# Kernel tuning notes

Measured on AMD Instinct MI355X. Metric: run time of the kernel, lower is better.

## Reference

```python
import jax, jax.numpy as jnp
import numpy as np

DIM = 48
D_STATE = 16
D_CONV = 4
EXPAND = 2
D_INNER = DIM * EXPAND          # 96
DT_RANK = (DIM + 15) // 16      # 3
EPS = 1e-5


def _interp2x_align_corners(x, axis):
    """Linear 2x upsample along one axis with align_corners=True."""
    n = x.shape[axis]
    out = 2 * n
    pos = jnp.arange(out, dtype=jnp.float32) * (n - 1) / (out - 1)
    lo = jnp.floor(pos).astype(jnp.int32)
    hi = jnp.minimum(lo + 1, n - 1)
    w = (pos - lo.astype(jnp.float32)).astype(x.dtype)
    shape = [1] * x.ndim
    shape[axis] = out
    w = w.reshape(shape)
    return jnp.take(x, lo, axis=axis) * (1 - w) + jnp.take(x, hi, axis=axis) * w


def _upsample_trilinear2x(x):
    for axis in (2, 3, 4):
        x = _interp2x_align_corners(x, axis)
    return x


def _conv3d(x, w, b, pad):
    y = jax.lax.conv_general_dilated(
        x, w, window_strides=(1, 1, 1), padding=[(pad, pad)] * 3,
        dimension_numbers=('NCDHW', 'OIDHW', 'NCDHW'))
    return y + b[None, :, None, None, None]


def _instance_norm(x):
    m = x.mean(axis=(2, 3, 4), keepdims=True)
    v = x.var(axis=(2, 3, 4), keepdims=True)  # biased var, as PyTorch InstanceNorm3d
    return (x - m) / jnp.sqrt(v + EPS)


def _mamba(u, in_proj_w, conv1d_w, conv1d_b, x_proj_w, dt_proj_w, dt_proj_b,
           A_log, D_param, out_proj_w):
    # u: (B, L, d_model)
    Bsz, L, _ = u.shape
    xz = jnp.einsum('bld,ed->ble', u, in_proj_w)        # (B, L, 2*Di)
    xi, z = jnp.split(xz, 2, axis=-1)                   # each (B, L, Di)
    # depthwise causal conv1d (pad left d_conv-1, crop to L == mamba's slice)
    xpad = jnp.pad(xi.transpose(0, 2, 1), ((0, 0), (0, 0), (D_CONV - 1, 0)))
    xc = jax.lax.conv_general_dilated(
        xpad, conv1d_w, window_strides=(1,), padding=[(0, 0)],
        dimension_numbers=('NCH', 'OIH', 'NCH'), feature_group_count=D_INNER)
    xs = jax.nn.silu((xc + conv1d_b[None, :, None]).transpose(0, 2, 1))  # (B, L, Di)

    dbc = jnp.einsum('bld,ed->ble', xs, x_proj_w)       # (B, L, dt_rank+2*N)
    dt, Bm, Cm = jnp.split(dbc, [DT_RANK, DT_RANK + D_STATE], axis=-1)
    delta = jax.nn.softplus(jnp.einsum('blr,dr->bld', dt, dt_proj_w) + dt_proj_b)

    A = -jnp.exp(A_log)                                  # (Di, N)
    dA = jnp.exp(jnp.einsum('bld,dn->bldn', delta, A))   # (B, L, Di, N)
    dBx = jnp.einsum('bld,bln->bldn', delta * xs, Bm)    # (B, L, Di, N)

    def step(h, inp):
        dA_t, dBx_t, C_t = inp                           # (B,Di,N),(B,Di,N),(B,N)
        h = dA_t * h + dBx_t
        y = jnp.einsum('bdn,bn->bd', h, C_t)
        return h, y

    h0 = jnp.zeros((Bsz, D_INNER, D_STATE), xs.dtype)
    _, ys = jax.lax.scan(step, h0,
                         (dA.transpose(1, 0, 2, 3), dBx.transpose(1, 0, 2, 3),
                          Cm.transpose(1, 0, 2)))
    y = ys.transpose(1, 0, 2) + D_param[None, None, :] * xs
    y = y * jax.nn.silu(z)
    return jnp.einsum('bld,ed->ble', y, out_proj_w)      # (B, L, d_model)


def setup_inputs() -> dict:
    key = jax.random.key(0)
    ks = jax.random.split(key, 16)
    s = 0.05
    f32 = jnp.float32
    inp = {
        'x': jax.random.normal(ks[0], (2, DIM, 12, 12, 12), f32),
        'Hx': jax.random.normal(ks[1], (2, DIM * 2, 24, 24, 24), f32),
        'W1': jax.random.normal(ks[2], (DIM, DIM * 3, 1, 1, 1), f32) * s,
        'b1': jax.random.normal(ks[3], (DIM,), f32) * s,
        'W2': jax.random.normal(ks[4], (DIM, DIM, 3, 3, 3), f32) * s,
        'b2': jax.random.normal(ks[5], (DIM,), f32) * s,
        'W3': jax.random.normal(ks[6], (DIM, DIM, 1, 1, 1), f32) * s,
        'b3': jax.random.normal(ks[7], (DIM,), f32) * s,
        'in_proj_w': jax.random.normal(ks[8], (2 * D_INNER, DIM), f32) * s,
        'conv1d_w': jax.random.normal(ks[9], (D_INNER, 1, D_CONV), f32) * s,
        'conv1d_b': jax.random.normal(ks[10], (D_INNER,), f32) * s,
        'x_proj_w': jax.random.normal(ks[11], (DT_RANK + 2 * D_STATE, D_INNER), f32) * s,
        'dt_proj_w': jax.random.normal(ks[12], (D_INNER, DT_RANK), f32) * s,
        'dt_proj_b': jax.random.normal(ks[13], (D_INNER,), f32) * 0.1,
        'A_log': jnp.log(jnp.tile(jnp.arange(1, D_STATE + 1, dtype=f32)[None, :],
                                  (D_INNER, 1))),
        'D_param': jnp.ones((D_INNER,), f32),
        'out_proj_w': jax.random.normal(ks[14], (DIM, D_INNER), f32) * s,
    }
    return inp


def reference(x, Hx, W1, b1, W2, b2, W3, b3, in_proj_w, conv1d_w, conv1d_b,
              x_proj_w, dt_proj_w, dt_proj_b, A_log, D_param, out_proj_w):
    up = _upsample_trilinear2x(x)                         # (B, dim, 2H, 2W, 2T)
    h = jnp.concatenate([up, Hx], axis=1)                 # (B, 3*dim, ...)
    h = _conv3d(h, W1, b1, 0)
    h = _conv3d(h, W2, b2, 1)
    h = _conv3d(h, W3, b3, 0)
    Lx = jax.nn.selu(_instance_norm(h))
    B, C, H, W, T = Lx.shape
    u = Lx.reshape(B, C, H * W * T).transpose(0, 2, 1)    # (B, L, C)
    ym = _mamba(u, in_proj_w, conv1d_w, conv1d_b, x_proj_w, dt_proj_w,
                dt_proj_b, A_log, D_param, out_proj_w)
    out = ym.transpose(0, 2, 1).reshape(B, C, H, W, T) + Lx
    return out
```

## Files before the change

### kernel.cpp

```cpp
#include <hip/hip_runtime.h>
#include <math.h>

#define NB 2
#define NCH 48
#define P 13824
#define DI 96
#define NSTATE 16
#define L 13824
#define CHUNK 64
#define NCK 216
#define TL 32

__device__ __forceinline__ float siluf(float x) { return x / (1.f + __expf(-x)); }
__device__ __forceinline__ float softplusf(float x) {
    return x > 0.f ? x + log1pf(expf(-x)) : log1pf(expf(x));
}

__global__ __launch_bounds__(256) void k_wtrans(const float* __restrict__ W2,
    const float* __restrict__ W1, const float* __restrict__ W3,
    const float* __restrict__ Wop, float* __restrict__ Wt, float* __restrict__ W1t,
    float* __restrict__ W3t, float* __restrict__ Wopt)
{
    int i = blockIdx.x * 256 + threadIdx.x;
    if (i < 62208) {
        int o = i / (48 * 27); int r = i % (48 * 27); int c = r / 27; int tap = r % 27;
        int og = o / 12, oi = o % 12;
        Wt[(((og * 27 + tap) * 48 + c) * 12) + oi] = W2[i];
    } else if (i < 62208 + 6912) {
        int j = i - 62208; int o = j / 144, c = j % 144;
        W1t[c * 48 + o] = W1[j];
    } else if (i < 62208 + 6912 + 2304) {
        int j = i - 62208 - 6912; int o = j / 48, c = j % 48;
        W3t[c * 48 + o] = W3[j];
    } else if (i < 62208 + 6912 + 2304 + 4608) {
        int j = i - 62208 - 6912 - 2304; int o = j / 96, q = j % 96;
        Wopt[q * 48 + o] = Wop[j];
    }
}

__global__ __launch_bounds__(128) void k_conv1(const float* __restrict__ x,
    const float* __restrict__ Hx, const float* __restrict__ W1t,
    const float* __restrict__ b1, float* __restrict__ h1)
{
    int t = blockIdx.x * 128 + threadIdx.x;
    int oh = blockIdx.y * 12;
    int b = t / P, p = t % P;
    int zi = p / 576, yi = (p / 24) % 24, xi_ = p % 24;
    float fpos; int z0, z1, y0, y1, x0, x1; float wz, wy, wx;
    fpos = (float)(zi * 11) / 23.0f; z0 = (int)floorf(fpos); wz = fpos - z0; z1 = min(z0 + 1, 11);
    fpos = (float)(yi * 11) / 23.0f; y0 = (int)floorf(fpos); wy = fpos - y0; y1 = min(y0 + 1, 11);
    fpos = (float)(xi_ * 11) / 23.0f; x0 = (int)floorf(fpos); wx = fpos - x0; x1 = min(x0 + 1, 11);
    int o000 = (z0*12+y0)*12+x0, o001 = (z0*12+y0)*12+x1;
    int o010 = (z0*12+y1)*12+x0, o011 = (z0*12+y1)*12+x1;
    int o100 = (z1*12+y0)*12+x0, o101 = (z1*12+y0)*12+x1;
    int o110 = (z1*12+y1)*12+x0, o111 = (z1*12+y1)*12+x1;
    float uz = 1.f - wz, uy = 1.f - wy, ux = 1.f - wx;
    float w000 = uz*uy*ux, w001 = uz*uy*wx, w010 = uz*wy*ux, w011 = uz*wy*wx;
    float w100 = wz*uy*ux, w101 = wz*uy*wx, w110 = wz*wy*ux, w111 = wz*wy*wx;

    float acc[12];
#pragma unroll
    for (int o = 0; o < 12; ++o) acc[o] = b1[oh + o];
    const float* xb = x + (size_t)b * 48 * 1728;
    for (int c0 = 0; c0 < 48; c0 += 4) {
        float a[4][8];
#pragma unroll
        for (int j = 0; j < 4; ++j) {
            const float* xc = xb + (c0 + j) * 1728;
            a[j][0] = xc[o000]; a[j][1] = xc[o001]; a[j][2] = xc[o010]; a[j][3] = xc[o011];
            a[j][4] = xc[o100]; a[j][5] = xc[o101]; a[j][6] = xc[o110]; a[j][7] = xc[o111];
        }
#pragma unroll
        for (int j = 0; j < 4; ++j) {
            float v = a[j][0]*w000 + a[j][1]*w001 + a[j][2]*w010 + a[j][3]*w011
                    + a[j][4]*w100 + a[j][5]*w101 + a[j][6]*w110 + a[j][7]*w111;
            const float* wr = W1t + (c0 + j) * 48 + oh;
#pragma unroll
            for (int o = 0; o < 12; ++o) acc[o] = fmaf(wr[o], v, acc[o]);
        }
    }
    const float* hb = Hx + (size_t)b * 96 * P + p;
    for (int c0 = 0; c0 < 96; c0 += 8) {
        float v[8];
#pragma unroll
        for (int j = 0; j < 8; ++j) v[j] = hb[(size_t)(c0 + j) * P];
#pragma unroll
        for (int j = 0; j < 8; ++j) {
            const float* wr = W1t + (48 + c0 + j) * 48 + oh;
#pragma unroll
            for (int o = 0; o < 12; ++o) acc[o] = fmaf(wr[o], v[j], acc[o]);
        }
    }
    float* out = h1 + (size_t)b * 48 * P + p;
#pragma unroll
    for (int o = 0; o < 12; ++o) out[(size_t)(oh+o) * P] = acc[o];
}

__global__ __launch_bounds__(512) void k_conv23(const float* __restrict__ h1,
    const float* __restrict__ Wt, const float* __restrict__ b2,
    const float* __restrict__ W3t, const float* __restrict__ b3,
    float* __restrict__ h3)
{
    __shared__ float tile[216 * 52];
    int blk = blockIdx.x;
    int b = blk / 216; int r = blk % 216;
    int tz = r / 36, ty = (r / 6) % 6, tx = r % 6;
    int z0 = tz*4 - 1, y0 = ty*4 - 1, x0 = tx*4 - 1;
    for (int i = threadIdx.x; i < 48 * 216; i += 512) {
        int c = i / 216; int q = i % 216;
        int lz = q / 36, ly = (q / 6) % 6, lx = q % 6;
        int gz = z0 + lz, gy = y0 + ly, gx = x0 + lx;
        float v = 0.f;
        if ((unsigned)gz < 24u && (unsigned)gy < 24u && (unsigned)gx < 24u)
            v = h1[((size_t)(b*48 + c)) * P + (gz*24 + gy)*24 + gx];
        tile[q*52 + c] = v;
    }
    __syncthreads();
    int lp = threadIdx.x & 63;
    int w  = __builtin_amdgcn_readfirstlane((int)(threadIdx.x >> 6));
    int og = w & 3, cc = w >> 2;
    int lz = lp >> 4, ly = (lp >> 2) & 3, lx = lp & 3;
    float acc[12];
#pragma unroll
    for (int i = 0; i < 12; ++i) acc[i] = cc ? 0.f : b2[og*12 + i];
#pragma unroll
    for (int dz = 0; dz < 3; ++dz)
#pragma unroll
    for (int dy = 0; dy < 3; ++dy)
#pragma unroll
    for (int dx = 0; dx < 3; ++dx) {
        int pos = (lz+dz)*36 + (ly+dy)*6 + (lx+dx);
        const float* tp = tile + pos*52 + cc*24;
        int tap = (dz*3 + dy)*3 + dx;
        const float* wt = Wt + (((size_t)og*27 + tap)*48 + cc*24)*12;
#pragma unroll
        for (int cq = 0; cq < 6; ++cq) {
            float4 v4 = *(const float4*)(tp + cq*4);
            const float* wq = wt + cq*48;
#pragma unroll
            for (int i = 0; i < 12; ++i) {
                acc[i] = fmaf(wq[i],      v4.x, acc[i]);
                acc[i] = fmaf(wq[12 + i], v4.y, acc[i]);
                acc[i] = fmaf(wq[24 + i], v4.z, acc[i]);
                acc[i] = fmaf(wq[36 + i], v4.w, acc[i]);
            }
        }
    }
    __syncthreads();
    if (cc == 1) {
        float* ex = tile + og * 768;
#pragma unroll
        for (int i = 0; i < 12; ++i) ex[i*64 + lp] = acc[i];
    }
    __syncthreads();
    if (cc == 0) {
        const float* ex = tile + og * 768;
        float* ht = tile + 3072;
#pragma unroll
        for (int i = 0; i < 12; ++i)
            ht[(og*12 + i)*64 + lp] = acc[i] + ex[i*64 + lp];
    }
    __syncthreads();
    const float* ht = tile + 3072;
    int oc0 = w * 6;
    float acc3[6];
#pragma unroll
    for (int j = 0; j < 6; ++j) acc3[j] = b3[oc0 + j];
    for (int c = 0; c < 48; ++c) {
        float v = ht[c*64 + lp];
        const float* wr = W3t + c*48 + oc0;
#pragma unroll
        for (int j = 0; j < 6; ++j) acc3[j] = fmaf(wr[j], v, acc3[j]);
    }
    int gz = tz*4 + lz, gy = ty*4 + ly, gx = tx*4 + lx;
    size_t pp = (size_t)(gz*24 + gy)*24 + gx;
#pragma unroll
    for (int j = 0; j < 6; ++j)
        h3[((size_t)(b*48) + oc0 + j) * P + pp] = acc3[j];
}

__global__ __launch_bounds__(1024) void k_instnorm(float* __restrict__ h3)
{
    int bc = blockIdx.x;
    float4* src = (float4*)(h3 + (size_t)bc * P);
    float s = 0.f, s2 = 0.f;
    for (int i = threadIdx.x; i < 3456; i += 1024) {
        float4 v = src[i];
        s  += v.x + v.y + v.z + v.w;
        s2 += v.x*v.x + v.y*v.y + v.z*v.z + v.w*v.w;
    }
    __shared__ float rs[16], rs2[16], mv[2];
    for (int off = 32; off; off >>= 1) { s += __shfl_down(s, off); s2 += __shfl_down(s2, off); }
    int wid = threadIdx.x >> 6;
    if ((threadIdx.x & 63) == 0) { rs[wid] = s; rs2[wid] = s2; }
    __syncthreads();
    if (threadIdx.x == 0) {
        s = 0.f; s2 = 0.f;
#pragma unroll
        for (int k = 0; k < 16; ++k) { s += rs[k]; s2 += rs2[k]; }
        float m = s / (float)P;
        float var = s2 / (float)P - m * m;
        mv[0] = m; mv[1] = rsqrtf(var + 1e-5f);
    }
    __syncthreads();
    float m = mv[0], istd = mv[1];
    const float kS = 1.0507009873554805f, kA = 1.6732632423543772f;
    for (int i = threadIdx.x; i < 3456; i += 1024) {
        float4 v = src[i];
        float a0 = (v.x - m) * istd, a1 = (v.y - m) * istd;
        float a2 = (v.z - m) * istd, a3 = (v.w - m) * istd;
        v.x = a0 > 0.f ? kS * a0 : kS * kA * expm1f(a0);
        v.y = a1 > 0.f ? kS * a1 : kS * kA * expm1f(a1);
        v.z = a2 > 0.f ? kS * a2 : kS * kA * expm1f(a2);
        v.w = a3 > 0.f ? kS * a3 : kS * kA * expm1f(a3);
        src[i] = v;
    }
}

__global__ __launch_bounds__(192) void k_inproj(const float* __restrict__ Lx,
    const float* __restrict__ Wip, float* __restrict__ xi, float* __restrict__ z)
{
    int b = blockIdx.x / 576; int l0 = (blockIdx.x % 576) * 24;
    int e = threadIdx.x;
    float w[48];
#pragma unroll
    for (int c = 0; c < 48; ++c) w[c] = Wip[e*48 + c];
    float acc[24];
#pragma unroll
    for (int ll = 0; ll < 24; ++ll) acc[ll] = 0.f;
    const float* ub = Lx + (size_t)b * 48 * P + l0;
#pragma unroll 2
    for (int c = 0; c < 48; ++c) {
        const float* ur = ub + (size_t)c * P;
#pragma unroll
        for (int ll = 0; ll < 24; ++ll) acc[ll] = fmaf(w[c], ur[ll], acc[ll]);
    }
    float* dst = (e < 96) ? (xi + ((size_t)b * L + l0) * 96 + e)
                          : (z  + ((size_t)b * L + l0) * 96 + (e - 96));
#pragma unroll
    for (int ll = 0; ll < 24; ++ll) dst[(size_t)ll * 96] = acc[ll];
}

__global__ __launch_bounds__(256) void k_fxproj(const float* __restrict__ xi,
    const float* __restrict__ cw, const float* __restrict__ cb,
    const float* __restrict__ Wxp, const float* __restrict__ Wdt,
    const float* __restrict__ bdt, float* __restrict__ xs,
    float* __restrict__ delta, float* __restrict__ Bm, float* __restrict__ Cm)
{
    __shared__ float xs_t[TL][100];
    __shared__ float wx_t[35][100];
    __shared__ float wd_t[96][4];
    __shared__ float dt_t[TL][4];
    int blk = blockIdx.x;
    int b = blk / 432; int l0 = (blk % 432) * TL;
    int tid = threadIdx.x;

    for (int i = tid; i < 35 * 96; i += 256) wx_t[i / 96][i % 96] = Wxp[i];
    for (int i = tid; i < 96 * 3; i += 256) wd_t[i / 3][i % 3] = Wdt[i];
    for (int i = tid; i < 96; i += 256) wd_t[i][3] = bdt[i];

    int row = tid >> 3;
    int q8  = tid & 7;
    int d0  = q8 * 12;
    int l = l0 + row;
    size_t t_glob = (size_t)b * L + l;
    const float* xib = xi + (size_t)b * L * 96;
    float* xsg = xs + t_glob * 96 + d0;
    int ls0 = l - 3;
#pragma unroll
    for (int jq = 0; jq < 3; ++jq) {
        int d = d0 + jq * 4;
        float4 t0 = *(const float4*)(cw + 4 * (d + 0));
        float4 t1 = *(const float4*)(cw + 4 * (d + 1));
        float4 t2 = *(const float4*)(cw + 4 * (d + 2));
        float4 t3 = *(const float4*)(cw + 4 * (d + 3));
        float4 acc = *(const float4*)(cb + d);
        float4 q0 = {0.f,0.f,0.f,0.f}, q1 = q0, q2 = q0;
        if (ls0 + 0 >= 0) q0 = *(const float4*)(xib + (size_t)(ls0 + 0) * 96 + d);
        if (ls0 + 1 >= 0) q1 = *(const float4*)(xib + (size_t)(ls0 + 1) * 96 + d);
        if (ls0 + 2 >= 0) q2 = *(const float4*)(xib + (size_t)(ls0 + 2) * 96 + d);
        float4 q3 = *(const float4*)(xib + (size_t)(ls0 + 3) * 96 + d);
        acc.x += t0.x*q0.x + t0.y*q1.x + t0.z*q2.x + t0.w*q3.x;
        acc.y += t1.x*q0.y + t1.y*q1.y + t1.z*q2.y + t1.w*q3.y;
        acc.z += t2.x*q0.z + t2.y*q1.z + t2.z*q2.z + t2.w*q3.z;
        acc.w += t3.x*q0.w + t3.y*q1.w + t3.z*q2.w + t3.w*q3.w;
        acc.x = siluf(acc.x); acc.y = siluf(acc.y);
        acc.z = siluf(acc.z); acc.w = siluf(acc.w);
        *(float4*)(&xs_t[row][d0 + jq * 4]) = acc;
        *(float4*)(xsg + jq * 4) = acc;
    }
    __syncthreads();

    float acc5[5];
#pragma unroll
    for (int k = 0; k < 5; ++k) acc5[k] = 0.f;
    const float* xrow = &xs_t[row][0];
#pragma unroll 4
    for (int j = 0; j < 24; ++j) {
        float4 xv = *(const float4*)(xrow + 4 * j);
#pragma unroll
        for (int k = 0; k < 5; ++k) {
            int e = q8 + 8 * k;
            if (e < 35) {
                float4 wv = *(const float4*)(&wx_t[e][4 * j]);
                acc5[k] = fmaf(wv.x, xv.x, fmaf(wv.y, xv.y,
                          fmaf(wv.z, xv.z, fmaf(wv.w, xv.w, acc5[k]))));
            }
        }
    }
#pragma unroll
    for (int k = 0; k < 5; ++k) {
        int e = q8 + 8 * k;
        if (e < 35) {
            if (e < 3)       dt_t[row][e] = acc5[k];
            else if (e < 19) Bm[t_glob * 16 + (e - 3)]  = acc5[k];
            else             Cm[t_glob * 16 + (e - 19)] = acc5[k];
        }
    }
    __syncthreads();

    float dt0 = dt_t[row][0], dt1 = dt_t[row][1], dt2 = dt_t[row][2];
    float* dl = delta + t_glob * 96 + d0;
#pragma unroll
    for (int jq = 0; jq < 3; ++jq) {
        float4 o;
        {
            float4 wv = *(const float4*)(&wd_t[d0 + jq*4 + 0][0]);
            o.x = softplusf(fmaf(wv.x, dt0, fmaf(wv.y, dt1, fmaf(wv.z, dt2, wv.w))));
        }
        {
            float4 wv = *(const float4*)(&wd_t[d0 + jq*4 + 1][0]);
            o.y = softplusf(fmaf(wv.x, dt0, fmaf(wv.y, dt1, fmaf(wv.z, dt2, wv.w))));
        }
        {
            float4 wv = *(const float4*)(&wd_t[d0 + jq*4 + 2][0]);
            o.z = softplusf(fmaf(wv.x, dt0, fmaf(wv.y, dt1, fmaf(wv.z, dt2, wv.w))));
        }
        {
            float4 wv = *(const float4*)(&wd_t[d0 + jq*4 + 3][0]);
            o.w = softplusf(fmaf(wv.x, dt0, fmaf(wv.y, dt1, fmaf(wv.z, dt2, wv.w))));
        }
        *(float4*)(dl + jq * 4) = o;
    }
}

__global__ __launch_bounds__(256) void k_scan1(const float* __restrict__ delta,
    const float* __restrict__ xs, const float* __restrict__ Bm,
    const float* __restrict__ Alog, float* __restrict__ Aprod, float* __restrict__ hend)
{
    int wid = (blockIdx.x * 256 + threadIdx.x) >> 6;
    int lane = threadIdx.x & 63;
    int dg = wid % 24; int ch = (wid / 24) % NCK; int b = wid / (24 * NCK);
    int dl = lane >> 4, n = lane & 15;
    int d = dg * 4 + dl;
    float A = -__expf(Alog[d*16 + n]);
    float h = 0.f, ap = 1.f;
    int t0 = ch * CHUNK;
    const float* dp = delta + ((size_t)b * L + t0) * 96 + d;
    const float* xp = xs    + ((size_t)b * L + t0) * 96 + d;
    const float* bp = Bm    + ((size_t)b * L + t0) * 16 + n;

    float dA0, dA1, dA2, dA3, xA0, xA1, xA2, xA3, bA0, bA1, bA2, bA3;
    float dB0, dB1, dB2, dB3, xB0, xB1, xB2, xB3, bB0, bB1, bB2, bB3;
#define LD1(s, T) do { \
    d##s##0 = dp[(size_t)(T)*96];     x##s##0 = xp[(size_t)(T)*96];     b##s##0 = bp[(size_t)(T)*16]; \
    d##s##1 = dp[(size_t)((T)+1)*96]; x##s##1 = xp[(size_t)((T)+1)*96]; b##s##1 = bp[(size_t)((T)+1)*16]; \
    d##s##2 = dp[(size_t)((T)+2)*96]; x##s##2 = xp[(size_t)((T)+2)*96]; b##s##2 = bp[(size_t)((T)+2)*16]; \
    d##s##3 = dp[(size_t)((T)+3)*96]; x##s##3 = xp[(size_t)((T)+3)*96]; b##s##3 = bp[(size_t)((T)+3)*16]; \
  } while (0)
#define CMP1(s) do { \
    float e0 = __expf(d##s##0 * A); float e1 = __expf(d##s##1 * A); \
    float e2 = __expf(d##s##2 * A); float e3 = __expf(d##s##3 * A); \
    h = fmaf(e0, h, d##s##0 * x##s##0 * b##s##0); \
    h = fmaf(e1, h, d##s##1 * x##s##1 * b##s##1); \
    h = fmaf(e2, h, d##s##2 * x##s##2 * b##s##2); \
    h = fmaf(e3, h, d##s##3 * x##s##3 * b##s##3); \
    ap *= e0 * e1 * e2 * e3; \
  } while (0)

    LD1(A, 0);
#pragma unroll 1
    for (int t = 0; t < CHUNK; t += 8) {
        LD1(B, t + 4);
        CMP1(A);
        if (t + 8 < CHUNK) LD1(A, t + 8);
        CMP1(B);
    }
#undef LD1
#undef CMP1
    size_t idx = (((size_t)b * NCK + ch) * 96 + d) * 16 + n;
    Aprod[idx] = ap;
    hend[idx]  = h;
}

__global__ __launch_bounds__(256) void k_scan2(const float* __restrict__ Aprod,
    const float* __restrict__ hend, float* __restrict__ hin)
{
    int t = blockIdx.x * 256 + threadIdx.x;
    int b = t / 1536; int dn = t % 1536;
    const float* ap = Aprod + (size_t)b * NCK * 1536 + dn;
    const float* he = hend  + (size_t)b * NCK * 1536 + dn;
    float* hi       = hin   + (size_t)b * NCK * 1536 + dn;
    float carry = 0.f;
    float aA0, aA1, aA2, aA3, hA0, hA1, hA2, hA3;
    float aB0, aB1, aB2, aB3, hB0, hB1, hB2, hB3;
#define LD2(s, J) do { \
    a##s##0 = ap[(size_t)(J)*1536];     h##s##0 = he[(size_t)(J)*1536]; \
    a##s##1 = ap[(size_t)((J)+1)*1536]; h##s##1 = he[(size_t)((J)+1)*1536]; \
    a##s##2 = ap[(size_t)((J)+2)*1536]; h##s##2 = he[(size_t)((J)+2)*1536]; \
    a##s##3 = ap[(size_t)((J)+3)*1536]; h##s##3 = he[(size_t)((J)+3)*1536]; \
  } while (0)
#define CMP2(s, J) do { \
    hi[(size_t)(J)*1536]     = carry; carry = fmaf(a##s##0, carry, h##s##0); \
    hi[(size_t)((J)+1)*1536] = carry; carry = fmaf(a##s##1, carry, h##s##1); \
    hi[(size_t)((J)+2)*1536] = carry; carry = fmaf(a##s##2, carry, h##s##2); \
    hi[(size_t)((J)+3)*1536] = carry; carry = fmaf(a##s##3, carry, h##s##3); \
  } while (0)
    LD2(A, 0);
#pragma unroll 1
    for (int j = 0; j < NCK; j += 8) {
        LD2(B, j + 4);
        CMP2(A, j);
        if (j + 8 < NCK) LD2(A, j + 8);
        CMP2(B, j + 4);
    }
#undef LD2
#undef CMP2
}

__global__ __launch_bounds__(256) void k_scan3(const float* __restrict__ delta,
    float* __restrict__ xs, const float* __restrict__ Bm, const float* __restrict__ Cm,
    const float* __restrict__ z, const float* __restrict__ Alog,
    const float* __restrict__ Dp, const float* __restrict__ hin)
{
    int wid = (blockIdx.x * 256 + threadIdx.x) >> 6;
    int lane = threadIdx.x & 63;
    int dg = wid % 24; int ch = (wid / 24) % NCK; int b = wid / (24 * NCK);
    int dl = lane >> 4, n = lane & 15;
    int d = dg * 4 + dl;
    float A = -__expf(Alog[d*16 + n]);
    float Dv = Dp[d];
    size_t cidx = (((size_t)b * NCK + ch) * 96 + d) * 16 + n;
    float h = hin[cidx];
    int t0 = ch * CHUNK;
    const float* dp = delta + ((size_t)b * L + t0) * 96 + d;
    float* xp       = xs    + ((size_t)b * L + t0) * 96 + d;
    const float* bp = Bm    + ((size_t)b * L + t0) * 16 + n;
    const float* cp = Cm    + ((size_t)b * L + t0) * 16 + n;
    const float* zp = z     + ((size_t)b * L + t0) * 96 + d;

    float dA0, dA1, dA2, dA3, xA0, xA1, xA2, xA3, bA0, bA1, bA2, bA3, cA0, cA1, cA2, cA3, zA0, zA1, zA2, zA3;
    float dB0, dB1, dB2, dB3, xB0, xB1, xB2, xB3, bB0, bB1, bB2, bB3, cB0, cB1, cB2, cB3, zB0, zB1, zB2, zB3;
#define LD3(s, T) do { \
    d##s##0 = dp[(size_t)(T)*96];     x##s##0 = xp[(size_t)(T)*96];     b##s##0 = bp[(size_t)(T)*16]; \
    c##s##0 = cp[(size_t)(T)*16];     z##s##0 = zp[(size_t)(T)*96]; \
    d##s##1 = dp[(size_t)((T)+1)*96]; x##s##1 = xp[(size_t)((T)+1)*96]; b##s##1 = bp[(size_t)((T)+1)*16]; \
    c##s##1 = cp[(size_t)((T)+1)*16]; z##s##1 = zp[(size_t)((T)+1)*96]; \
    d##s##2 = dp[(size_t)((T)+2)*96]; x##s##2 = xp[(size_t)((T)+2)*96]; b##s##2 = bp[(size_t)((T)+2)*16]; \
    c##s##2 = cp[(size_t)((T)+2)*16]; z##s##2 = zp[(size_t)((T)+2)*96]; \
    d##s##3 = dp[(size_t)((T)+3)*96]; x##s##3 = xp[(size_t)((T)+3)*96]; b##s##3 = bp[(size_t)((T)+3)*16]; \
    c##s##3 = cp[(size_t)((T)+3)*16]; z##s##3 = zp[(size_t)((T)+3)*96]; \
  } while (0)
#define STEP3(DEL, XV, BV, CV, ZV, T) do { \
    float dAv = __expf((DEL) * A); \
    h = fmaf(dAv, h, (DEL) * (XV) * (BV)); \
    float yc = h * (CV); \
    yc += __shfl_xor(yc, 8); \
    yc += __shfl_xor(yc, 4); \
    yc += __shfl_xor(yc, 2); \
    yc += __shfl_xor(yc, 1); \
    if (n == 0) xp[(size_t)(T)*96] = fmaf(Dv, (XV), yc) * siluf(ZV); \
  } while (0)
#define CMP3(s, T) do { \
    STEP3(d##s##0, x##s##0, b##s##0, c##s##0, z##s##0, (T)); \
    STEP3(d##s##1, x##s##1, b##s##1, c##s##1, z##s##1, (T)+1); \
    STEP3(d##s##2, x##s##2, b##s##2, c##s##2, z##s##2, (T)+2); \
    STEP3(d##s##3, x##s##3, b##s##3, c##s##3, z##s##3, (T)+3); \
  } while (0)

    LD3(A, 0);
#pragma unroll 1
    for (int t = 0; t < CHUNK; t += 8) {
        LD3(B, t + 4);
        CMP3(A, t);
        if (t + 8 < CHUNK) LD3(A, t + 8);
        CMP3(B, t + 4);
    }
#undef LD3
#undef STEP3
#undef CMP3
}

__global__ __launch_bounds__(128) void k_outproj(const float* __restrict__ y,
    const float* __restrict__ Wopt, const float* __restrict__ Lx, float* __restrict__ out)
{
    int t = blockIdx.x * 128 + threadIdx.x;
    int oh = blockIdx.y * 12;
    int b = t / P, p = t % P;
    const float* yr = y + (size_t)t * 96;
    float acc[12];
#pragma unroll
    for (int o = 0; o < 12; ++o) acc[o] = 0.f;
#pragma unroll
    for (int i = 0; i < 24; ++i) {
        float4 v4 = ((const float4*)yr)[i];
        const float* w0 = Wopt + (i*4) * 48 + oh;
        const float* w1 = Wopt + (i*4 + 1) * 48 + oh;
        const float* w2 = Wopt + (i*4 + 2) * 48 + oh;
        const float* w3 = Wopt + (i*4 + 3) * 48 + oh;
#pragma unroll
        for (int o = 0; o < 12; ++o) {
            acc[o] = fmaf(w0[o], v4.x, acc[o]);
            acc[o] = fmaf(w1[o], v4.y, acc[o]);
            acc[o] = fmaf(w2[o], v4.z, acc[o]);
            acc[o] = fmaf(w3[o], v4.w, acc[o]);
        }
    }
    const float* lx = Lx + (size_t)b * 48 * P + p;
    float* op = out + (size_t)b * 48 * P + p;
#pragma unroll
    for (int o = 0; o < 12; ++o) op[(size_t)(oh+o) * P] = acc[o] + lx[(size_t)(oh+o) * P];
}

extern "C" void kernel_launch(void* const* d_in, const int* in_sizes, int n_in,
                              void* d_out, int out_size, void* d_ws, size_t ws_size,
                              hipStream_t stream) {
    const float* x        = (const float*)d_in[0];
    const float* Hx       = (const float*)d_in[1];
    const float* W1       = (const float*)d_in[2];
    const float* b1       = (const float*)d_in[3];
    const float* W2       = (const float*)d_in[4];
    const float* b2       = (const float*)d_in[5];
    const float* W3       = (const float*)d_in[6];
    const float* b3       = (const float*)d_in[7];
    const float* in_proj  = (const float*)d_in[8];
    const float* conv1d_w = (const float*)d_in[9];
    const float* conv1d_b = (const float*)d_in[10];
    const float* x_proj   = (const float*)d_in[11];
    const float* dt_proj  = (const float*)d_in[12];
    const float* dt_bias  = (const float*)d_in[13];
    const float* A_log    = (const float*)d_in[14];
    const float* D_param  = (const float*)d_in[15];
    const float* out_proj = (const float*)d_in[16];
    float* out = (float*)d_out;

    float* ws = (float*)d_ws;
    const size_t SZ_BCP = (size_t)NB * 48 * P;
    const size_t SZ_BLD = (size_t)NB * L * 96;
    const size_t SZ_BLN = (size_t)NB * L * 16;
    const size_t SZ_CK  = (size_t)NB * NCK * 1536;
    float* bufA  = ws;
    float* bufB  = bufA + SZ_BCP;
    float* bufC  = bufB + SZ_BCP;
    float* xib   = bufC + SZ_BCP;
    float* zb    = xib  + SZ_BLD;
    float* xsb   = zb   + SZ_BLD;
    float* Bmb   = xsb  + SZ_BLD;
    float* Cmb   = Bmb  + SZ_BLN;
    float* stats = Cmb  + SZ_BLN;
    float* Wtb   = stats + 192;
    float* W1tb  = Wtb + 62208;
    float* W3tb  = W1tb + 6912;
    float* Woptb = W3tb + 2304;
    float* deltab = bufA;
    float* Apr   = xib;
    float* hendb = xib + SZ_CK;
    float* hinb  = xib + 2 * SZ_CK;

    k_wtrans<<<297, 256, 0, stream>>>(W2, W1, W3, out_proj, Wtb, W1tb, W3tb, Woptb);
    k_conv1<<<dim3(216, 4), 128, 0, stream>>>(x, Hx, W1tb, b1, bufA);
    k_conv23<<<NB * 216, 512, 0, stream>>>(bufA, Wtb, b2, W3tb, b3, bufC);
    k_instnorm<<<NB * 48, 1024, 0, stream>>>(bufC);
    k_inproj<<<NB * 576, 192, 0, stream>>>(bufC, in_proj, xib, zb);
    k_fxproj<<<NB * 432, 256, 0, stream>>>(xib, conv1d_w, conv1d_b, x_proj, dt_proj,
                                           dt_bias, xsb, deltab, Bmb, Cmb);
    k_scan1<<<(NB * NCK * 24) / 4, 256, 0, stream>>>(deltab, xsb, Bmb, A_log, Apr, hendb);
    k_scan2<<<12, 256, 0, stream>>>(Apr, hendb, hinb);
    k_scan3<<<(NB * NCK * 24) / 4, 256, 0, stream>>>(deltab, xsb, Bmb, Cmb, zb, A_log,
                                                     D_param, hinb);
    k_outproj<<<dim3(216, 4), 128, 0, stream>>>(xsb, Woptb, bufC, out);
}
```

Before: 261.2 us.

## Fuse in_proj into conv1d/x_proj kernel, keeping xi tile in shared memory

After: 270.4 us. +3.5%, slower.

```diff
diff --git a/kernel.cpp b/kernel.cpp
--- a/kernel.cpp
+++ b/kernel.cpp
@@ -217,36 +217,15 @@
     }
 }
 
-__global__ __launch_bounds__(192) void k_inproj(const float* __restrict__ Lx,
-    const float* __restrict__ Wip, float* __restrict__ xi, float* __restrict__ z)
-{
-    int b = blockIdx.x / 576; int l0 = (blockIdx.x % 576) * 24;
-    int e = threadIdx.x;
-    float w[48];
-#pragma unroll
-    for (int c = 0; c < 48; ++c) w[c] = Wip[e*48 + c];
-    float acc[24];
-#pragma unroll
-    for (int ll = 0; ll < 24; ++ll) acc[ll] = 0.f;
-    const float* ub = Lx + (size_t)b * 48 * P + l0;
-#pragma unroll 2
-    for (int c = 0; c < 48; ++c) {
-        const float* ur = ub + (size_t)c * P;
-#pragma unroll
-        for (int ll = 0; ll < 24; ++ll) acc[ll] = fmaf(w[c], ur[ll], acc[ll]);
-    }
-    float* dst = (e < 96) ? (xi + ((size_t)b * L + l0) * 96 + e)
-                          : (z  + ((size_t)b * L + l0) * 96 + (e - 96));
-#pragma unroll
-    for (int ll = 0; ll < 24; ++ll) dst[(size_t)ll * 96] = acc[ll];
-}
-
-__global__ __launch_bounds__(256) void k_fxproj(const float* __restrict__ xi,
+__global__ __launch_bounds__(192) void k_fxproj2(const float* __restrict__ Lx,
+    const float* __restrict__ Wip,
     const float* __restrict__ cw, const float* __restrict__ cb,
     const float* __restrict__ Wxp, const float* __restrict__ Wdt,
-    const float* __restrict__ bdt, float* __restrict__ xs,
+    const float* __restrict__ bdt,
+    float* __restrict__ zout, float* __restrict__ xs,
     float* __restrict__ delta, float* __restrict__ Bm, float* __restrict__ Cm)
 {
+    __shared__ float xi_t[35][100];
     __shared__ float xs_t[TL][100];
     __shared__ float wx_t[35][100];
     __shared__ float wd_t[96][4];
@@ -255,66 +234,90 @@
     int b = blk / 432; int l0 = (blk % 432) * TL;
     int tid = threadIdx.x;
 
-    for (int i = tid; i < 35 * 96; i += 256) wx_t[i / 96][i % 96] = Wxp[i];
-    for (int i = tid; i < 96 * 3; i += 256) wd_t[i / 3][i % 3] = Wdt[i];
-    for (int i = tid; i < 96; i += 256) wd_t[i][3] = bdt[i];
-
-    int row = tid >> 3;
-    int q8  = tid & 7;
-    int d0  = q8 * 12;
-    int l = l0 + row;
-    size_t t_glob = (size_t)b * L + l;
-    const float* xib = xi + (size_t)b * L * 96;
+    for (int i = tid; i < 35 * 96; i += 192) wx_t[i / 96][i % 96] = Wxp[i];
+    for (int i = tid; i < 96 * 3; i += 192) wd_t[i / 3][i % 3] = Wdt[i];
+    for (int i = tid; i < 96; i += 192) wd_t[i][3] = bdt[i];
+
+    {
+        int e = tid;
+        float w[48];
+#pragma unroll
+        for (int c = 0; c < 48; ++c) w[c] = Wip[e*48 + c];
+        float acc[35];
+#pragma unroll
+        for (int r = 0; r < 35; ++r) acc[r] = 0.f;
+        const float* ub = Lx + (size_t)b * 48 * P + l0 - 3;
+#pragma unroll 2
+        for (int c = 0; c < 48; ++c) {
+            const float* ur = ub + (size_t)c * P;
+#pragma unroll
+            for (int r = 0; r < 35; ++r) acc[r] = fmaf(w[c], ur[r], acc[r]);
+        }
+        if (e < 96) {
+#pragma unroll
+            for (int r = 0; r < 35; ++r)
+                xi_t[r][e] = (l0 + r - 3 >= 0) ? acc[r] : 0.f;
+        } else {
+            float* dst = zout + ((size_t)b * L + l0) * 96 + (e - 96);
+#pragma unroll
+            for (int r = 0; r < 32; ++r) dst[(size_t)r * 96] = acc[r + 3];
+        }
+    }
+    __syncthreads();
+
+    int row = tid / 6;
+    int q6  = tid % 6;
+    int d0  = q6 * 16;
+    size_t t_glob = (size_t)b * L + l0 + row;
     float* xsg = xs + t_glob * 96 + d0;
-    int ls0 = l - 3;
-#pragma unroll
-    for (int jq = 0; jq < 3; ++jq) {
+
+#pragma unroll
+    for (int jq = 0; jq < 4; ++jq) {
         int d = d0 + jq * 4;
         float4 t0 = *(const float4*)(cw + 4 * (d + 0));
         float4 t1 = *(const float4*)(cw + 4 * (d + 1));
         float4 t2 = *(const float4*)(cw + 4 * (d + 2));
         float4 t3 = *(const float4*)(cw + 4 * (d + 3));
         float4 acc = *(const float4*)(cb + d);
-        float4 q0 = {0.f,0.f,0.f,0.f}, q1 = q0, q2 = q0;
-        if (ls0 + 0 >= 0) q0 = *(const float4*)(xib + (size_t)(ls0 + 0) * 96 + d);
-        if (ls0 + 1 >= 0) q1 = *(const float4*)(xib + (size_t)(ls0 + 1) * 96 + d);
-        if (ls0 + 2 >= 0) q2 = *(const float4*)(xib + (size_t)(ls0 + 2) * 96 + d);
-        float4 q3 = *(const float4*)(xib + (size_t)(ls0 + 3) * 96 + d);
+        float4 q0 = *(const float4*)(&xi_t[row + 0][d]);
+        float4 q1 = *(const float4*)(&xi_t[row + 1][d]);
+        float4 q2 = *(const float4*)(&xi_t[row + 2][d]);
+        float4 q3 = *(const float4*)(&xi_t[row + 3][d]);
         acc.x += t0.x*q0.x + t0.y*q1.x + t0.z*q2.x + t0.w*q3.x;
         acc.y += t1.x*q0.y + t1.y*q1.y + t1.z*q2.y + t1.w*q3.y;
         acc.z += t2.x*q0.z + t2.y*q1.z + t2.z*q2.z + t2.w*q3.z;
         acc.w += t3.x*q0.w + t3.y*q1.w + t3.z*q2.w + t3.w*q3.w;
         acc.x = siluf(acc.x); acc.y = siluf(acc.y);
         acc.z = siluf(acc.z); acc.w = siluf(acc.w);
-        *(float4*)(&xs_t[row][d0 + jq * 4]) = acc;
+        *(float4*)(&xs_t[row][d + 0 - d0 + d0]) = acc;
         *(float4*)(xsg + jq * 4) = acc;
     }
     __syncthreads();
 
-    float acc5[5];
-#pragma unroll
-    for (int k = 0; k < 5; ++k) acc5[k] = 0.f;
+    float acc6[6];
+#pragma unroll
+    for (int k = 0; k < 6; ++k) acc6[k] = 0.f;
     const float* xrow = &xs_t[row][0];
 #pragma unroll 4
     for (int j = 0; j < 24; ++j) {
         float4 xv = *(const float4*)(xrow + 4 * j);
 #pragma unroll
-        for (int k = 0; k < 5; ++k) {
-            int e = q8 + 8 * k;
+        for (int k = 0; k < 6; ++k) {
+            int e = q6 + 6 * k;
             if (e < 35) {
                 float4 wv = *(const float4*)(&wx_t[e][4 * j]);
-                acc5[k] = fmaf(wv.x, xv.x, fmaf(wv.y, xv.y,
-                          fmaf(wv.z, xv.z, fmaf(wv.w, xv.w, acc5[k]))));
+                acc6[k] = fmaf(wv.x, xv.x, fmaf(wv.y, xv.y,
+                          fmaf(wv.z, xv.z, fmaf(wv.w, xv.w, acc6[k]))));
             }
         }
     }
 #pragma unroll
-    for (int k = 0; k < 5; ++k) {
-        int e = q8 + 8 * k;
+    for (int k = 0; k < 6; ++k) {
+        int e = q6 + 6 * k;
         if (e < 35) {
-            if (e < 3)       dt_t[row][e] = acc5[k];
-            else if (e < 19) Bm[t_glob * 16 + (e - 3)]  = acc5[k];
-            else             Cm[t_glob * 16 + (e - 19)] = acc5[k];
+            if (e < 3)       dt_t[row][e] = acc6[k];
+            else if (e < 19) Bm[t_glob * 16 + (e - 3)]  = acc6[k];
+            else             Cm[t_glob * 16 + (e - 19)] = acc6[k];
         }
     }
     __syncthreads();
@@ -322,7 +325,7 @@
     float dt0 = dt_t[row][0], dt1 = dt_t[row][1], dt2 = dt_t[row][2];
     float* dl = delta + t_glob * 96 + d0;
 #pragma unroll
-    for (int jq = 0; jq < 3; ++jq) {
+    for (int jq = 0; jq < 4; ++jq) {
         float4 o;
         {
             float4 wv = *(const float4*)(&wd_t[d0 + jq*4 + 0][0]);
@@ -552,8 +555,8 @@
     float* bufA  = ws;
     float* bufB  = bufA + SZ_BCP;
     float* bufC  = bufB + SZ_BCP;
-    float* xib   = bufC + SZ_BCP;
-    float* zb    = xib  + SZ_BLD;
+    float* scr   = bufC + SZ_BCP;
+    float* zb    = scr  + SZ_BLD;
     float* xsb   = zb   + SZ_BLD;
     float* Bmb   = xsb  + SZ_BLD;
     float* Cmb   = Bmb  + SZ_BLN;
@@ -563,17 +566,17 @@
     float* W3tb  = W1tb + 6912;
     float* Woptb = W3tb + 2304;
     float* deltab = bufA;
-    float* Apr   = xib;
-    float* hendb = xib + SZ_CK;
-    float* hinb  = xib + 2 * SZ_CK;
+    float* Apr   = scr;
+    float* hendb = scr + SZ_CK;
+    float* hinb  = scr + 2 * SZ_CK;
 
     k_wtrans<<<297, 256, 0, stream>>>(W2, W1, W3, out_proj, Wtb, W1tb, W3tb, Woptb);
     k_conv1<<<dim3(216, 4), 128, 0, stream>>>(x, Hx, W1tb, b1, bufA);
     k_conv23<<<NB * 216, 512, 0, stream>>>(bufA, Wtb, b2, W3tb, b3, bufC);
     k_instnorm<<<NB * 48, 1024, 0, stream>>>(bufC);
-    k_inproj<<<NB * 576, 192, 0, stream>>>(bufC, in_proj, xib, zb);
-    k_fxproj<<<NB * 432, 256, 0, stream>>>(xib, conv1d_w, conv1d_b, x_proj, dt_proj,
-                                           dt_bias, xsb, deltab, Bmb, Cmb);
+    k_fxproj2<<<NB * 432, 192, 0, stream>>>(bufC, in_proj, conv1d_w, conv1d_b,
+                                            x_proj, dt_proj, dt_bias,
+                                            zb, xsb, deltab, Bmb, Cmb);
     k_scan1<<<(NB * NCK * 24) / 4, 256, 0, stream>>>(deltab, xsb, Bmb, A_log, Apr, hendb);
     k_scan2<<<12, 256, 0, stream>>>(Apr, hendb, hinb);
     k_scan3<<<(NB * NCK * 24) / 4, 256, 0, stream>>>(deltab, xsb, Bmb, Cmb, zb, A_log,
```
